# Performance work log

Hardware: AMD Instinct MI355X
Metric: run time of the kernel (lower is better)

## Reference

```python
import jax, jax.numpy as jnp
import numpy as np

B, N, A, O, D, Q, H = 64, 4, 1024, 128, 256, 256, 128
NEG_INF = -1e30


def setup_inputs() -> dict:
    key = jax.random.key(0)
    ks = jax.random.split(key, 8)
    q = jax.random.normal(ks[0], (B, N, 1, Q), dtype=jnp.float32)
    att1 = jax.random.uniform(ks[1], (B, N, A, O), dtype=jnp.float32)
    obj_reps = jax.random.normal(ks[2], (B, O, D), dtype=jnp.float32)
    tags_attention = jax.random.randint(ks[3], (B, N, A), 0, 2, dtype=jnp.int32)
    W1 = jax.random.normal(ks[4], (D + Q, H), dtype=jnp.float32) / np.sqrt(D + Q)
    b1 = jnp.zeros((H,), dtype=jnp.float32)
    W2 = jax.random.normal(ks[5], (H, 1), dtype=jnp.float32) / np.sqrt(H)
    b2 = jnp.zeros((1,), dtype=jnp.float32)
    return {"q": q, "att1": att1, "obj_reps": obj_reps,
            "tags_attention": tags_attention,
            "W1": W1, "b1": b1, "W2": W2, "b2": b2, "t": 1}


def reference(q, att1, obj_reps, tags_attention, W1, b1, W2, b2, t):
    # v: [B,N,A,D] = att1 [B,N,A,O] @ obj_reps [B,O,D]
    v = jnp.einsum('bnao,bod->bnad', att1, obj_reps)
    # q broadcast over token dim A, concat -> [B,N,A,D+Q]
    q_proj = jnp.broadcast_to(q, v.shape[:3] + (q.shape[-1],))
    vq = jnp.concatenate([v, q_proj], axis=-1)
    # FCNet: Linear + ReLU (dropout is identity at inference)
    joint_repr = jax.nn.relu(vq @ W1 + b1)          # [B,N,A,H]
    logits = (joint_repr @ W2 + b2)[..., 0]          # [B,N,A]
    # temperature-scaled masked softmax over tokens
    masked = jnp.where(tags_attention > 0, logits / t, NEG_INF)
    att2 = jax.nn.softmax(masked, axis=-1)           # [B,N,A]
    # attention_last: [B,N,O] = att2 [B,N,1,A] @ att1 [B,N,A,O]
    return jnp.einsum('bna,bnao->bno', att2, att1)
```

## Files before the change

kernel.cpp:

```cpp
#include <hip/hip_runtime.h>
#include <math.h>

#define Bc 64
#define Nc 4
#define Ac 1024
#define Oc 128
#define Dc 256
#define Qc 256
#define Hc 128
#define BN (Bc*Nc)

using f4     = __attribute__((ext_vector_type(4))) float;
using f32x4  = __attribute__((ext_vector_type(4))) float;
using short8 = __attribute__((ext_vector_type(8))) short;
using us4    = __attribute__((ext_vector_type(4))) unsigned short;

__device__ inline float decode_t(const void* p) {
    int i = *(const int*)p;
    if (i >= 1 && i <= 1000000) return (float)i;
    return __int_as_float(i);
}

__device__ inline unsigned short bf16_rne(float x) {
    unsigned u = __builtin_bit_cast(unsigned, x);
    u += 0x7FFFu + ((u >> 16) & 1u);
    return (unsigned short)(u >> 16);
}

__device__ inline void split_bf16(float x, unsigned short& hi, unsigned short& lo) {
    unsigned u = __builtin_bit_cast(unsigned, x);
    hi = (unsigned short)(u >> 16);
    float hif = __builtin_bit_cast(float, u & 0xFFFF0000u);
    float lof = x - hif;
    lo = (unsigned short)(__builtin_bit_cast(unsigned, lof) >> 16);
}

__global__ __launch_bounds__(256) void prep_M_kernel(
    const float* __restrict__ obj, const float* __restrict__ W1,
    unsigned short* __restrict__ Mt_hi, unsigned short* __restrict__ Mt_lo)
{
    __shared__ float w_s[32][36];
    __shared__ float obj_sT[32][68];

    const int t  = threadIdx.x;
    const int tx = t & 15;
    const int ty = t >> 4;
    const int h0 = blockIdx.x * 32;
    const int o0 = blockIdx.y * 64;
    const int b  = blockIdx.z;
    const int r8 = t >> 3, c8 = t & 7;

    const float* objb = obj + ((size_t)b * Oc + o0) * Dc;

    float acc[2][4];
    #pragma unroll
    for (int i = 0; i < 2; i++)
        #pragma unroll
        for (int j = 0; j < 4; j++) acc[i][j] = 0.f;

    f4 wv  = *(const f4*)(W1 + (size_t)r8 * Hc + h0 + c8 * 4);
    f4 ov0 = *(const f4*)(objb + (size_t)r8 * Dc + c8 * 4);
    f4 ov1 = *(const f4*)(objb + (size_t)(r8 + 32) * Dc + c8 * 4);

    for (int ko = 0; ko < 8; ++ko) {
        *(f4*)&w_s[r8][c8 * 4] = wv;
        obj_sT[c8 * 4 + 0][r8] = ov0[0];
        obj_sT[c8 * 4 + 1][r8] = ov0[1];
        obj_sT[c8 * 4 + 2][r8] = ov0[2];
        obj_sT[c8 * 4 + 3][r8] = ov0[3];
        obj_sT[c8 * 4 + 0][r8 + 32] = ov1[0];
        obj_sT[c8 * 4 + 1][r8 + 32] = ov1[1];
        obj_sT[c8 * 4 + 2][r8 + 32] = ov1[2];
        obj_sT[c8 * 4 + 3][r8 + 32] = ov1[3];
        __syncthreads();
        if (ko < 7) {
            wv  = *(const f4*)(W1 + (size_t)((ko + 1) * 32 + r8) * Hc + h0 + c8 * 4);
            ov0 = *(const f4*)(objb + (size_t)r8 * Dc + (ko + 1) * 32 + c8 * 4);
            ov1 = *(const f4*)(objb + (size_t)(r8 + 32) * Dc + (ko + 1) * 32 + c8 * 4);
        }
        #pragma unroll 4
        for (int k = 0; k < 32; k++) {
            float a0 = w_s[k][ty * 2];
            float a1 = w_s[k][ty * 2 + 1];
            f4 bv = *(const f4*)&obj_sT[k][tx * 4];
            #pragma unroll
            for (int j = 0; j < 4; j++) {
                acc[0][j] += a0 * bv[j];
                acc[1][j] += a1 * bv[j];
            }
        }
        __syncthreads();
    }

    #pragma unroll
    for (int i = 0; i < 2; i++) {
        us4 hi, lo;
        #pragma unroll
        for (int j = 0; j < 4; j++) {
            unsigned short h16, l16;
            split_bf16(acc[i][j], h16, l16);
            hi[j] = h16; lo[j] = l16;
        }
        size_t ofs = ((size_t)b * Hc + h0 + ty * 2 + i) * Oc + o0 + tx * 4;
        *(us4*)(Mt_hi + ofs) = hi;
        *(us4*)(Mt_lo + ofs) = lo;
    }
}

__global__ __launch_bounds__(512) void prep_qb_kernel(
    const float* __restrict__ q, const float* __restrict__ W1,
    const float* __restrict__ b1, float* __restrict__ qb)
{
    __shared__ float qs[256];
    __shared__ float red[4][128];
    const int t = threadIdx.x;
    const int bn = blockIdx.x;

    if (t < 256) qs[t] = q[bn * Qc + t];
    __syncthreads();

    const int h = t & 127, kq = t >> 7;
    float acc = 0.f;
    const float* w = W1 + (size_t)(Dc + kq * 64) * Hc + h;
    #pragma unroll 8
    for (int d = 0; d < 64; ++d)
        acc += qs[kq * 64 + d] * w[(size_t)d * Hc];
    red[kq][h] = acc;
    __syncthreads();

    if (t < 128)
        qb[bn * Hc + t] = b1[t] + red[0][t] + red[1][t] + red[2][t] + red[3][t];
}

__global__ __launch_bounds__(512, 4) void main_half_kernel(
    const float* __restrict__ att1, const int* __restrict__ tags,
    const unsigned short* __restrict__ Mt_hi, const unsigned short* __restrict__ Mt_lo,
    const float* __restrict__ qb, const float* __restrict__ W2,
    const float* __restrict__ b2, const void* __restrict__ tptr,
    float* __restrict__ out_part, float* __restrict__ z_part)
{
    __shared__ unsigned short A_s[64][136];
    __shared__ float part2[64][9];
    __shared__ float part3[4][132];
    __shared__ float e_s[64];
    __shared__ float qb_s[128], w2_s[128];

    const int t    = threadIdx.x;
    const int lane = t & 63;
    const int wave = t >> 6;
    const int l15  = lane & 15;
    const int quad = lane >> 4;
    const int blk  = blockIdx.x;
    const int bn   = blk >> 1;
    const int half = blk & 1;
    const int b    = bn >> 2;
    const int hw   = wave * 16;

    const float* att_half = att1 + ((size_t)bn * Ac + half * 512) * Oc;

    f4 sv[4];
    #pragma unroll
    for (int s = 0; s < 4; s++) {
        int idx = t + 512 * s;
        sv[s] = *(const f4*)(att_half + (size_t)idx * 4);
    }

    const size_t brow = ((size_t)b * Hc + hw + l15) * Oc;
    short8 Bh[4], Bl[4];
    #pragma unroll
    for (int ks = 0; ks < 4; ks++) {
        const int ko = ks * 32 + quad * 8;
        Bh[ks] = *(const short8*)(Mt_hi + brow + ko);
        Bl[ks] = *(const short8*)(Mt_lo + brow + ko);
    }

    if (t < 128) { qb_s[t] = qb[bn * Hc + t]; w2_s[t] = W2[t]; }
    int tg_cur = (t < 64) ? tags[(size_t)bn * Ac + half * 512 + t] : 0;
    const float b2v  = b2[0];
    const float tval = decode_t(tptr);

    float z_reg = 0.f, out_reg = 0.f;

    for (int tile = 0; tile < 8; ++tile) {
        const float* tile_ptr = att_half + (size_t)tile * 64 * Oc;

        if (tile > 0 && t < 128) {
            float s = 0.f;
            #pragma unroll
            for (int g = 0; g < 4; g++) s += part3[g][t];
            out_reg += s;
        }
        #pragma unroll
        for (int s = 0; s < 4; s++) {
            int idx = t + 512 * s;
            int r = idx >> 5, c4 = idx & 31;
            us4 h4;
            #pragma unroll
            for (int j = 0; j < 4; j++) h4[j] = bf16_rne(sv[s][j]);
            *(us4*)&A_s[r][c4 * 4] = h4;
        }
        __syncthreads();

        int tg_next = 0;
        if (tile < 7) {
            const float* np = tile_ptr + 64 * Oc;
            #pragma unroll
            for (int s = 0; s < 4; s++) {
                int idx = t + 512 * s;
                sv[s] = *(const f4*)(np + (size_t)idx * 4);
            }
            if (t < 64) tg_next = tags[(size_t)bn * Ac + half * 512 + (tile + 1) * 64 + t];
        }

        f32x4 acc[4];
        #pragma unroll
        for (int i = 0; i < 4; i++) acc[i] = (f32x4)(0.f);
        #pragma unroll
        for (int ks = 0; ks < 4; ks++) {
            const int ko = ks * 32 + quad * 8;
            #pragma unroll
            for (int i = 0; i < 4; i++) {
                short8 ah = *(const short8*)&A_s[i * 16 + l15][ko];
                acc[i] = __builtin_amdgcn_mfma_f32_16x16x32_bf16(ah, Bh[ks], acc[i], 0, 0, 0);
                acc[i] = __builtin_amdgcn_mfma_f32_16x16x32_bf16(ah, Bl[ks], acc[i], 0, 0, 0);
            }
        }

        {
            const float qbv = qb_s[hw + l15], w2v = w2_s[hw + l15];
            float p[4][4];
            #pragma unroll
            for (int i = 0; i < 4; i++)
                #pragma unroll
                for (int r = 0; r < 4; r++) {
                    float v = acc[i][r] + qbv;
                    v = v > 0.f ? v : 0.f;
                    p[i][r] = v * w2v;
                }
            #pragma unroll
            for (int m = 1; m <= 8; m <<= 1)
                #pragma unroll
                for (int i = 0; i < 4; i++)
                    #pragma unroll
                    for (int r = 0; r < 4; r++)
                        p[i][r] += __shfl_xor(p[i][r], m);
            if (l15 == 0) {
                #pragma unroll
                for (int i = 0; i < 4; i++)
                    #pragma unroll
                    for (int r = 0; r < 4; r++)
                        part2[i * 16 + quad * 4 + r][wave] = p[i][r];
            }
        }
        __syncthreads();

        if (t < 64) {
            float sum = b2v;
            #pragma unroll
            for (int x = 0; x < 8; x++) sum += part2[t][x];
            float logit = sum / tval;
            float e = (tg_cur > 0) ? __expf(logit) : 0.f;
            e_s[t] = e;
            z_reg += e;
        }
        __syncthreads();

        {
            const int o = t & 127;
            const int g = t >> 7;
            const float* ab = tile_ptr + (size_t)(g * 16) * Oc + o;
            float accum = 0.f;
            #pragma unroll
            for (int a = 0; a < 16; a++)
                accum += e_s[g * 16 + a] * ab[(size_t)a * Oc];
            part3[g][o] = accum;
        }
        __syncthreads();
        tg_cur = tg_next;
    }

    if (t < 128) {
        float s = 0.f;
        #pragma unroll
        for (int g = 0; g < 4; g++) s += part3[g][t];
        out_reg += s;
        out_part[(size_t)blk * 128 + t] = out_reg;
    }
    if (t < 64) {
        float z = z_reg;
        #pragma unroll
        for (int off = 32; off > 0; off >>= 1) z += __shfl_down(z, off);
        if (t == 0) z_part[blk] = z;
    }
}

__global__ __launch_bounds__(128) void finalize_kernel(
    const float* __restrict__ out_part, const float* __restrict__ z_part,
    float* __restrict__ out)
{
    const int bn = blockIdx.x;
    const int t  = threadIdx.x;
    const float Z = z_part[bn * 2] + z_part[bn * 2 + 1];
    const float v = out_part[(size_t)(bn * 2) * 128 + t]
                  + out_part[(size_t)(bn * 2 + 1) * 128 + t];
    out[(size_t)bn * 128 + t] = v / Z;
}

extern "C" void kernel_launch(void* const* d_in, const int* in_sizes, int n_in,
                              void* d_out, int out_size, void* d_ws, size_t ws_size,
                              hipStream_t stream)
{
    (void)in_sizes; (void)n_in; (void)out_size; (void)ws_size;

    const float* q    = (const float*)d_in[0];
    const float* att1 = (const float*)d_in[1];
    const float* obj  = (const float*)d_in[2];
    const int*   tags = (const int*)d_in[3];
    const float* W1   = (const float*)d_in[4];
    const float* b1   = (const float*)d_in[5];
    const float* W2   = (const float*)d_in[6];
    const float* b2   = (const float*)d_in[7];
    const void*  tptr = (const void*)d_in[8];
    float* out = (float*)d_out;

    char* wsb = (char*)d_ws;
    unsigned short* Mt_hi = (unsigned short*)wsb;
    unsigned short* Mt_lo = (unsigned short*)(wsb + (size_t)2*1024*1024);
    float* qbuf     = (float*)(wsb + (size_t)4*1024*1024);
    float* out_part = (float*)(wsb + (size_t)5*1024*1024);
    float* z_part   = (float*)(wsb + (size_t)6*1024*1024);

    prep_M_kernel<<<dim3(4, 2, Bc), 256, 0, stream>>>(obj, W1, Mt_hi, Mt_lo);
    prep_qb_kernel<<<dim3(BN), 512, 0, stream>>>(q, W1, b1, qbuf);
    main_half_kernel<<<dim3(2 * BN), 512, 0, stream>>>(att1, tags, Mt_hi, Mt_lo,
                                                       qbuf, W2, b2, tptr,
                                                       out_part, z_part);
    finalize_kernel<<<dim3(BN), 128, 0, stream>>>(out_part, z_part, out);
}
```

Before: 242.7 us.

## Compute obj@W1 precompute with split-bf16 MFMA and reuse att1 tile from LDS

The scalar FP32 LDS-tiled GEMM that built M = obj·W1 is replaced by a pre-pass that splits obj and a transposed W1 into bf16 hi/lo pairs, followed by a kernel that does the product with bf16 MFMA using four hi/lo cross terms to keep near-fp32 accuracy. Separately, the main kernel now also stores each fp32 att1 tile in shared memory so the final att2·att1 reduction reads it from LDS instead of re-reading global memory. This adds an extra launch, extra workspace traffic for the split copies, and a larger LDS footprint that may reduce occupancy of the main kernel.

```diff
diff --git a/kernel.cpp b/kernel.cpp
--- a/kernel.cpp
+++ b/kernel.cpp
@@ -35,75 +35,98 @@
     lo = (unsigned short)(__builtin_bit_cast(unsigned, lof) >> 16);
 }
 
-__global__ __launch_bounds__(256) void prep_M_kernel(
+__global__ __launch_bounds__(256) void prep_split_kernel(
     const float* __restrict__ obj, const float* __restrict__ W1,
+    unsigned short* __restrict__ obj_hi, unsigned short* __restrict__ obj_lo,
+    unsigned short* __restrict__ W1T_hi, unsigned short* __restrict__ W1T_lo)
+{
+    __shared__ float Ts[64][65];
+    const int t = threadIdx.x;
+    const int bid = blockIdx.x;
+
+    if (bid < 1024) {
+        size_t i0 = ((size_t)bid * 256 + t) * 8;
+        f4 v0 = *(const f4*)(obj + i0);
+        f4 v1 = *(const f4*)(obj + i0 + 4);
+        short8 hi, lo;
+        unsigned short h16, l16;
+        #pragma unroll
+        for (int j = 0; j < 4; j++) {
+            split_bf16(v0[j], h16, l16); hi[j] = (short)h16; lo[j] = (short)l16;
+        }
+        #pragma unroll
+        for (int j = 0; j < 4; j++) {
+            split_bf16(v1[j], h16, l16); hi[4 + j] = (short)h16; lo[4 + j] = (short)l16;
+        }
+        *(short8*)(obj_hi + i0) = hi;
+        *(short8*)(obj_lo + i0) = lo;
+    } else {
+        const int wb = bid - 1024;
+        const int d0 = (wb & 3) * 64, h0 = (wb >> 2) * 64;
+        const int r4 = t >> 6, c = t & 63;
+        #pragma unroll
+        for (int rr = 0; rr < 16; rr++) {
+            int d = rr * 4 + r4;
+            Ts[d][c] = W1[(size_t)(d0 + d) * Hc + h0 + c];
+        }
+        __syncthreads();
+        #pragma unroll
+        for (int rr = 0; rr < 16; rr++) {
+            int hl = rr * 4 + r4;
+            float v = Ts[c][hl];
+            unsigned short h16, l16;
+            split_bf16(v, h16, l16);
+            W1T_hi[(size_t)(h0 + hl) * Dc + d0 + c] = h16;
+            W1T_lo[(size_t)(h0 + hl) * Dc + d0 + c] = l16;
+        }
+    }
+}
+
+__global__ __launch_bounds__(256, 4) void prep_M2_kernel(
+    const unsigned short* __restrict__ W1T_hi, const unsigned short* __restrict__ W1T_lo,
+    const unsigned short* __restrict__ obj_hi, const unsigned short* __restrict__ obj_lo,
     unsigned short* __restrict__ Mt_hi, unsigned short* __restrict__ Mt_lo)
 {
-    __shared__ float w_s[32][36];
-    __shared__ float obj_sT[32][68];
-
-    const int t  = threadIdx.x;
-    const int tx = t & 15;
-    const int ty = t >> 4;
-    const int h0 = blockIdx.x * 32;
-    const int o0 = blockIdx.y * 64;
+    const int t = threadIdx.x;
+    const int wave = t >> 6, lane = t & 63;
+    const int l15 = lane & 15, quad = lane >> 4;
+    const int h0 = blockIdx.x * 64 + wave * 16;
+    const int o0 = blockIdx.y * 32;
     const int b  = blockIdx.z;
-    const int r8 = t >> 3, c8 = t & 7;
-
-    const float* objb = obj + ((size_t)b * Oc + o0) * Dc;
-
-    float acc[2][4];
+
+    const size_t arow  = (size_t)(h0 + l15) * Dc;
+    const size_t brow0 = ((size_t)b * Oc + o0 + l15) * Dc;
+    const size_t brow1 = ((size_t)b * Oc + o0 + 16 + l15) * Dc;
+
+    f32x4 acc0 = (f32x4)(0.f), acc1 = (f32x4)(0.f);
     #pragma unroll
-    for (int i = 0; i < 2; i++)
-        #pragma unroll
-        for (int j = 0; j < 4; j++) acc[i][j] = 0.f;
-
-    f4 wv  = *(const f4*)(W1 + (size_t)r8 * Hc + h0 + c8 * 4);
-    f4 ov0 = *(const f4*)(objb + (size_t)r8 * Dc + c8 * 4);
-    f4 ov1 = *(const f4*)(objb + (size_t)(r8 + 32) * Dc + c8 * 4);
-
-    for (int ko = 0; ko < 8; ++ko) {
-        *(f4*)&w_s[r8][c8 * 4] = wv;
-        obj_sT[c8 * 4 + 0][r8] = ov0[0];
-        obj_sT[c8 * 4 + 1][r8] = ov0[1];
-        obj_sT[c8 * 4 + 2][r8] = ov0[2];
-        obj_sT[c8 * 4 + 3][r8] = ov0[3];
-        obj_sT[c8 * 4 + 0][r8 + 32] = ov1[0];
-        obj_sT[c8 * 4 + 1][r8 + 32] = ov1[1];
-        obj_sT[c8 * 4 + 2][r8 + 32] = ov1[2];
-        obj_sT[c8 * 4 + 3][r8 + 32] = ov1[3];
-        __syncthreads();
-        if (ko < 7) {
-            wv  = *(const f4*)(W1 + (size_t)((ko + 1) * 32 + r8) * Hc + h0 + c8 * 4);
-            ov0 = *(const f4*)(objb + (size_t)r8 * Dc + (ko + 1) * 32 + c8 * 4);
-            ov1 = *(const f4*)(objb + (size_t)(r8 + 32) * Dc + (ko + 1) * 32 + c8 * 4);
-        }
-        #pragma unroll 4
-        for (int k = 0; k < 32; k++) {
-            float a0 = w_s[k][ty * 2];
-            float a1 = w_s[k][ty * 2 + 1];
-            f4 bv = *(const f4*)&obj_sT[k][tx * 4];
-            #pragma unroll
-            for (int j = 0; j < 4; j++) {
-                acc[0][j] += a0 * bv[j];
-                acc[1][j] += a1 * bv[j];
-            }
-        }
-        __syncthreads();
+    for (int ks = 0; ks < 8; ks++) {
+        const int ko = ks * 32 + quad * 8;
+        short8 Ah  = *(const short8*)(W1T_hi + arow + ko);
+        short8 Al  = *(const short8*)(W1T_lo + arow + ko);
+        short8 B0h = *(const short8*)(obj_hi + brow0 + ko);
+        short8 B0l = *(const short8*)(obj_lo + brow0 + ko);
+        short8 B1h = *(const short8*)(obj_hi + brow1 + ko);
+        short8 B1l = *(const short8*)(obj_lo + brow1 + ko);
+        acc0 = __builtin_amdgcn_mfma_f32_16x16x32_bf16(Al, B0l, acc0, 0, 0, 0);
+        acc0 = __builtin_amdgcn_mfma_f32_16x16x32_bf16(Al, B0h, acc0, 0, 0, 0);
+        acc0 = __builtin_amdgcn_mfma_f32_16x16x32_bf16(Ah, B0l, acc0, 0, 0, 0);
+        acc0 = __builtin_amdgcn_mfma_f32_16x16x32_bf16(Ah, B0h, acc0, 0, 0, 0);
+        acc1 = __builtin_amdgcn_mfma_f32_16x16x32_bf16(Al, B1l, acc1, 0, 0, 0);
+        acc1 = __builtin_amdgcn_mfma_f32_16x16x32_bf16(Al, B1h, acc1, 0, 0, 0);
+        acc1 = __builtin_amdgcn_mfma_f32_16x16x32_bf16(Ah, B1l, acc1, 0, 0, 0);
+        acc1 = __builtin_amdgcn_mfma_f32_16x16x32_bf16(Ah, B1h, acc1, 0, 0, 0);
     }
 
     #pragma unroll
-    for (int i = 0; i < 2; i++) {
-        us4 hi, lo;
-        #pragma unroll
-        for (int j = 0; j < 4; j++) {
-            unsigned short h16, l16;
-            split_bf16(acc[i][j], h16, l16);
-            hi[j] = h16; lo[j] = l16;
-        }
-        size_t ofs = ((size_t)b * Hc + h0 + ty * 2 + i) * Oc + o0 + tx * 4;
-        *(us4*)(Mt_hi + ofs) = hi;
-        *(us4*)(Mt_lo + ofs) = lo;
+    for (int r = 0; r < 4; r++) {
+        int hrow = h0 + quad * 4 + r;
+        size_t base = ((size_t)b * Hc + hrow) * Oc + o0 + l15;
+        unsigned short hh, ll;
+        split_bf16(acc0[r], hh, ll);
+        Mt_hi[base] = hh; Mt_lo[base] = ll;
+        split_bf16(acc1[r], hh, ll);
+        Mt_hi[base + 16] = hh; Mt_lo[base + 16] = ll;
     }
 }
 
@@ -140,6 +163,7 @@
     float* __restrict__ out_part, float* __restrict__ z_part)
 {
     __shared__ unsigned short A_s[64][136];
+    __shared__ float A32_s[64][132];
     __shared__ float part2[64][9];
     __shared__ float part3[4][132];
     __shared__ float e_s[64];
@@ -182,8 +206,6 @@
     float z_reg = 0.f, out_reg = 0.f;
 
     for (int tile = 0; tile < 8; ++tile) {
-        const float* tile_ptr = att_half + (size_t)tile * 64 * Oc;
-
         if (tile > 0 && t < 128) {
             float s = 0.f;
             #pragma unroll
@@ -198,12 +220,13 @@
             #pragma unroll
             for (int j = 0; j < 4; j++) h4[j] = bf16_rne(sv[s][j]);
             *(us4*)&A_s[r][c4 * 4] = h4;
+            *(f4*)&A32_s[r][c4 * 4] = sv[s];
         }
         __syncthreads();
 
         int tg_next = 0;
         if (tile < 7) {
-            const float* np = tile_ptr + 64 * Oc;
+            const float* np = att_half + (size_t)(tile + 1) * 64 * Oc;
             #pragma unroll
             for (int s = 0; s < 4; s++) {
                 int idx = t + 512 * s;
@@ -268,11 +291,10 @@
         {
             const int o = t & 127;
             const int g = t >> 7;
-            const float* ab = tile_ptr + (size_t)(g * 16) * Oc + o;
             float accum = 0.f;
             #pragma unroll
             for (int a = 0; a < 16; a++)
-                accum += e_s[g * 16 + a] * ab[(size_t)a * Oc];
+                accum += e_s[g * 16 + a] * A32_s[g * 16 + a][o];
             part3[g][o] = accum;
         }
         __syncthreads();
@@ -324,13 +346,20 @@
     float* out = (float*)d_out;
 
     char* wsb = (char*)d_ws;
-    unsigned short* Mt_hi = (unsigned short*)wsb;
-    unsigned short* Mt_lo = (unsigned short*)(wsb + (size_t)2*1024*1024);
-    float* qbuf     = (float*)(wsb + (size_t)4*1024*1024);
-    float* out_part = (float*)(wsb + (size_t)5*1024*1024);
-    float* z_part   = (float*)(wsb + (size_t)6*1024*1024);
-
-    prep_M_kernel<<<dim3(4, 2, Bc), 256, 0, stream>>>(obj, W1, Mt_hi, Mt_lo);
+    unsigned short* Mt_hi  = (unsigned short*)wsb;
+    unsigned short* Mt_lo  = (unsigned short*)(wsb + (size_t) 2*1024*1024);
+    float* qbuf            = (float*)         (wsb + (size_t) 4*1024*1024);
+    float* out_part        = (float*)         (wsb + (size_t) 5*1024*1024);
+    float* z_part          = (float*)         (wsb + (size_t) 6*1024*1024);
+    unsigned short* W1T_hi = (unsigned short*)(wsb + (size_t) 7*1024*1024);
+    unsigned short* W1T_lo = (unsigned short*)(wsb + (size_t) 7*1024*1024 + 64*1024);
+    unsigned short* obj_hi = (unsigned short*)(wsb + (size_t) 8*1024*1024);
+    unsigned short* obj_lo = (unsigned short*)(wsb + (size_t)12*1024*1024);
+
+    prep_split_kernel<<<dim3(1032), 256, 0, stream>>>(obj, W1, obj_hi, obj_lo,
+                                                      W1T_hi, W1T_lo);
+    prep_M2_kernel<<<dim3(2, 4, Bc), 256, 0, stream>>>(W1T_hi, W1T_lo, obj_hi, obj_lo,
+                                                       Mt_hi, Mt_lo);
     prep_qb_kernel<<<dim3(BN), 512, 0, stream>>>(q, W1, b1, qbuf);
     main_half_kernel<<<dim3(2 * BN), 512, 0, stream>>>(att1, tags, Mt_hi, Mt_lo,
                                                        qbuf, W2, b2, tptr,
```

Result: no change. 245.7 us (+1.2%).
